# Kernel tuning notes

Measured on AMD Instinct MI355X. Metric: run time of the kernel, lower is better.

Reference implementation:

```python
import jax, jax.numpy as jnp
import numpy as np

D_IN = 32
D_MODEL = 128
B, T = 512, 512
INPUT_DIM = 2 * D_IN  # concat_mask=True, d_u=0


def setup_inputs() -> dict:
    key = jax.random.key(0)
    ks = jax.random.split(key, 8)
    scale = 0.05
    return {
        "x": jax.random.normal(ks[0], (B, T, D_IN), dtype=jnp.float32),
        "W_ih": jax.random.normal(ks[1], (3 * D_MODEL, INPUT_DIM), dtype=jnp.float32) * scale,
        "W_hh": jax.random.normal(ks[2], (3 * D_MODEL, D_MODEL), dtype=jnp.float32) * scale,
        "b_ih": jax.random.normal(ks[3], (3 * D_MODEL,), dtype=jnp.float32) * scale,
        "b_hh": jax.random.normal(ks[4], (3 * D_MODEL,), dtype=jnp.float32) * scale,
        "W_out": jax.random.normal(ks[5], (D_IN, D_MODEL), dtype=jnp.float32) * scale,
        "b_out": jax.random.normal(ks[6], (D_IN,), dtype=jnp.float32) * scale,
        "mask": jax.random.randint(ks[7], (B, T, D_IN), 0, 2, dtype=jnp.int32),
    }


def reference(x, W_ih, W_hh, b_ih, b_hh, W_out, b_out, mask):
    m_bool = mask.astype(bool)                      # [B,T,d_in]
    m_f = mask.astype(x.dtype)
    x = jnp.where(m_bool, x, jnp.zeros_like(x))     # zero-fill missing

    h0 = jnp.zeros((x.shape[0], D_MODEL), dtype=x.dtype)   # state_init='zero'
    x_hat0 = h0 @ W_out.T + b_out                   # readout of initial state

    def gru_cell(x_t, h):
        gx = x_t @ W_ih.T + b_ih                    # [B, 3*d_model]
        gh = h @ W_hh.T + b_hh
        xr, xz, xn = jnp.split(gx, 3, axis=-1)
        hr, hz, hn = jnp.split(gh, 3, axis=-1)
        r = jax.nn.sigmoid(xr + hr)
        z = jax.nn.sigmoid(xz + hz)
        n = jnp.tanh(xn + r * hn)
        return (1.0 - z) * n + z * h

    def step(carry, inp):
        h, x_hat = carry
        x_s, mb_s, mf_s = inp                       # [B,d_in] each
        x_p = jnp.where(mb_s, x_s, x_hat)           # fill blanks with prediction
        x_t = jnp.concatenate([x_p, mf_s], axis=-1) # concat_mask=True
        h_new = gru_cell(x_t, h)
        x_hat_new = h_new @ W_out.T + b_out
        return (h_new, x_hat_new), x_hat_new

    # scan over steps 0..T-2 (time-major)
    xs = jnp.swapaxes(x[:, :-1], 0, 1)              # [T-1, B, d_in]
    mbs = jnp.swapaxes(m_bool[:, :-1], 0, 1)
    mfs = jnp.swapaxes(m_f[:, :-1], 0, 1)
    _, preds = jax.lax.scan(step, (h0, x_hat0), (xs, mbs, mfs))  # [T-1, B, d_in]

    out = jnp.concatenate([x_hat0[None], preds], axis=0)         # [T, B, d_in]
    return jnp.swapaxes(out, 0, 1)                                # [B, T, d_in]
```

## Files before the change

### kernel.cpp

```cpp
#include <hip/hip_runtime.h>
#include <hip/hip_bf16.h>

#define D_IN 32
#define TT 512
#define GB 16
#define NBLK 32
#define MAGIC 0x51F7C0DEu

typedef __attribute__((ext_vector_type(8))) short bf16x8;
typedef __attribute__((ext_vector_type(4))) float f32x4;
typedef __attribute__((ext_vector_type(4))) int   i32x4;
typedef __attribute__((ext_vector_type(2))) unsigned u32x2;

__device__ inline short bf16_of(float f) {
    union { float f; unsigned u; } v; v.f = f;
    unsigned r = v.u + 0x7FFFu + ((v.u >> 16) & 1u);
    return (short)(r >> 16);
}
__device__ inline unsigned cvt_pk_bf16(float lo, float hi) {
    unsigned r;
    asm("v_cvt_pk_bf16_f32 %0, %1, %2" : "=v"(r) : "v"(lo), "v"(hi));
    return r;
}
__device__ inline bf16x8 load8_bf16(const float* __restrict__ p) {
    bf16x8 r;
#pragma unroll
    for (int e = 0; e < 8; ++e) r[e] = bf16_of(p[e]);
    return r;
}
__device__ inline bf16x8 load44_bf16(const float* __restrict__ p, int qq) {
    bf16x8 r;
#pragma unroll
    for (int e = 0; e < 4; ++e) {
        r[e]     = bf16_of(p[qq * 4 + e]);
        r[4 + e] = bf16_of(p[16 + qq * 4 + e]);
    }
    return r;
}
__device__ inline f32x4 splat4(float v) { return (f32x4){v, v, v, v}; }

__device__ inline float sigmoid_fast(float x) {
    return __builtin_amdgcn_rcpf(1.0f + __expf(-x));
}
__device__ inline float tanh_fast(float x) {
    return 1.0f - 2.0f * __builtin_amdgcn_rcpf(__expf(2.0f * x) + 1.0f);
}
__device__ inline void lds_barrier() {
    asm volatile("s_waitcnt lgkmcnt(0)\n\ts_barrier" ::: "memory");
}

__global__ __launch_bounds__(512, 2)
void rnn_imputer(const float* __restrict__ x,
                 const float* __restrict__ W_ih,
                 const float* __restrict__ W_hh,
                 const float* __restrict__ b_ih,
                 const float* __restrict__ b_hh,
                 const float* __restrict__ W_out,
                 const float* __restrict__ b_out,
                 const int*   __restrict__ mask,
                 float* __restrict__ out,
                 unsigned*    flags,
                 int          use_spin) {
    if (blockIdx.x >= NBLK) {
        if (!use_spin || threadIdx.x >= 64) return;
        const unsigned long long t0 = __builtin_amdgcn_s_memrealtime();
        float a0 = 1.0f + threadIdx.x * 1e-6f, a1 = a0 + 0.1f, a2 = a0 + 0.2f,
              a3 = a0 + 0.3f, a4 = a0 + 0.4f, a5 = a0 + 0.5f, a6 = a0 + 0.6f,
              a7 = a0 + 0.7f;
        for (;;) {
            unsigned acc = 0;
#pragma unroll
            for (int j = 0; j < NBLK; ++j)
                acc |= (__hip_atomic_load(&flags[j], __ATOMIC_RELAXED,
                                          __HIP_MEMORY_SCOPE_AGENT) ^ MAGIC);
            if (acc == 0) break;
            if (__builtin_amdgcn_s_memrealtime() - t0 > 200000ull) break;
            for (int i = 0; i < 32; ++i) {
                a0 = __builtin_fmaf(a0, 1.0000001f, 1e-8f);
                a1 = __builtin_fmaf(a1, 1.0000001f, 1e-8f);
                a2 = __builtin_fmaf(a2, 1.0000001f, 1e-8f);
                a3 = __builtin_fmaf(a3, 1.0000001f, 1e-8f);
                a4 = __builtin_fmaf(a4, 1.0000001f, 1e-8f);
                a5 = __builtin_fmaf(a5, 1.0000001f, 1e-8f);
                a6 = __builtin_fmaf(a6, 1.0000001f, 1e-8f);
                a7 = __builtin_fmaf(a7, 1.0000001f, 1e-8f);
            }
            __builtin_amdgcn_s_sleep(24);
        }
        const float s = a0 + a1 + a2 + a3 + a4 + a5 + a6 + a7;
        if (s == 1.2345e30f) ((float*)flags)[NBLK + 1] = s;
        return;
    }

    __shared__ __align__(16) float xch[16][GB][36];
    __shared__ __align__(16) int   mch[16][GB][36];
    __shared__ __align__(16) short hbuf[2][GB][136];
    __shared__ __align__(16) unsigned a0sh[4][16][4];
    __shared__ __align__(16) unsigned a1sh[4][16][4];

    const int tid  = threadIdx.x;
    const int wv   = tid >> 6;
    const int lane = tid & 63;
    const int q    = lane >> 4;
    const int c    = lane & 15;
    const int bb   = blockIdx.x * GB;
    const int brow = bb + c;
    const int i_col = wv * 16 + c;

    bf16x8 Br[6], Bz[6], Bxn[2], Bhn[4];
    Br[0]  = load44_bf16(W_ih + (size_t)i_col * 64, q);
    Br[1]  = load44_bf16(W_ih + (size_t)i_col * 64 + 32, q);
    Bz[0]  = load44_bf16(W_ih + (size_t)(128 + i_col) * 64, q);
    Bz[1]  = load44_bf16(W_ih + (size_t)(128 + i_col) * 64 + 32, q);
    Bxn[0] = load44_bf16(W_ih + (size_t)(256 + i_col) * 64, q);
    Bxn[1] = load44_bf16(W_ih + (size_t)(256 + i_col) * 64 + 32, q);
#pragma unroll
    for (int kt = 2; kt < 6; ++kt) {
        const int k = (kt - 2) * 32 + q * 8;
        Br[kt] = load8_bf16(W_hh + (size_t)i_col * 128 + k);
        Bz[kt] = load8_bf16(W_hh + (size_t)(128 + i_col) * 128 + k);
    }
#pragma unroll
    for (int kt = 0; kt < 4; ++kt)
        Bhn[kt] = load8_bf16(W_hh + (size_t)(256 + i_col) * 128 + kt * 32 + q * 8);

    bf16x8 Ao[2][4];
#pragma unroll
    for (int ta = 0; ta < 2; ++ta)
#pragma unroll
        for (int kt = 0; kt < 4; ++kt)
            Ao[ta][kt] = load8_bf16(W_out + (size_t)(ta * 16 + c) * 128 + kt * 32 + q * 8);

    f32x4 bo_v[2];
#pragma unroll
    for (int ta = 0; ta < 2; ++ta)
        bo_v[ta] = *(const f32x4*)&b_out[ta * 16 + q * 4];

    const float bR  = b_ih[i_col]       + b_hh[i_col];
    const float bZ  = b_ih[128 + i_col] + b_hh[128 + i_col];
    const float bXN = b_ih[256 + i_col];
    const float bHN = b_hh[256 + i_col];

    float h_reg[4] = {0.f, 0.f, 0.f, 0.f};

    bf16x8 A0, A1;
    {
        const size_t o = (size_t)brow * TT * D_IN;
        const f32x4 xa = *(const f32x4*)&x[o + q * 4];
        const f32x4 xb = *(const f32x4*)&x[o + 16 + q * 4];
        const i32x4 ma = *(const i32x4*)&mask[o + q * 4];
        const i32x4 mb = *(const i32x4*)&mask[o + 16 + q * 4];
        union { bf16x8 v; unsigned d[4]; } a0, a1;
#pragma unroll
        for (int j = 0; j < 4; ++j) {
            const float fa = ma[j] ? xa[j] : b_out[q * 4 + j];
            const float fb = mb[j] ? xb[j] : b_out[16 + q * 4 + j];
            ((short*)&a0.v)[j]     = bf16_of(fa);
            ((short*)&a0.v)[4 + j] = bf16_of(fb);
            ((short*)&a1.v)[j]     = ma[j] ? (short)0x3F80 : (short)0;
            ((short*)&a1.v)[4 + j] = mb[j] ? (short)0x3F80 : (short)0;
        }
        A0 = a0.v; A1 = a1.v;
    }
#pragma unroll
    for (int ta = 0; ta < 2; ++ta)
        if (wv == ta)
            *(f32x4*)&out[(size_t)brow * TT * D_IN + ta * 16 + q * 4] = bo_v[ta];

#pragma unroll
    for (int rnd = 0; rnd < 4; ++rnd) {
        const int ts  = 1 + rnd * 4 + (tid >> 7);
        const int row = (tid >> 3) & 15;
        const int c4  = (tid & 7) * 4;
        const size_t o = ((size_t)(bb + row) * TT + ts) * D_IN + c4;
        *(f32x4*)&xch[ts & 15][row][c4] = *(const f32x4*)&x[o];
        *(i32x4*)&mch[ts & 15][row][c4] = *(const i32x4*)&mask[o];
    }

    f32x4 Ra = splat4(bR), Za = splat4(bZ);
    f32x4 Rb = splat4(0.f), Zb = splat4(0.f);
    f32x4 HNa = splat4(bHN), HNb = splat4(0.f);

    f32x4 sgx[2] = {splat4(0.f), splat4(0.f)};
    i32x4 sgm[2] = {(i32x4){0,0,0,0}, (i32x4){0,0,0,0}};

    __syncthreads();

    for (int t = 0; t < TT - 1; ++t) {
        Rb = __builtin_amdgcn_mfma_f32_16x16x32_bf16(A0, Br[0],  Rb, 0, 0, 0);
        Zb = __builtin_amdgcn_mfma_f32_16x16x32_bf16(A0, Bz[0],  Zb, 0, 0, 0);
        f32x4 XNb = __builtin_amdgcn_mfma_f32_16x16x32_bf16(A0, Bxn[0], splat4(0.f), 0, 0, 0);
        Ra = __builtin_amdgcn_mfma_f32_16x16x32_bf16(A1, Br[1],  Ra, 0, 0, 0);
        Za = __builtin_amdgcn_mfma_f32_16x16x32_bf16(A1, Bz[1],  Za, 0, 0, 0);
        f32x4 XNa = __builtin_amdgcn_mfma_f32_16x16x32_bf16(A1, Bxn[1], splat4(bXN), 0, 0, 0);

        const int sl = (t + 1) & 15;
        f32x4 pfx = splat4(0.f);
        i32x4 pfm = (i32x4){0, 0, 0, 0};
        if (wv < 2) {
            pfx = *(const f32x4*)&xch[sl][c][wv * 16 + q * 4];
            pfm = *(const i32x4*)&mch[sl][c][wv * 16 + q * 4];
        }

        if ((t & 7) == 0 && t) {
#pragma unroll
            for (int rnd = 0; rnd < 2; ++rnd) {
                const int tsu = t + 8 + rnd * 4 + (tid >> 7);
                const int row = (tid >> 3) & 15;
                const int c4  = (tid & 7) * 4;
                *(f32x4*)&xch[tsu & 15][row][c4] = sgx[rnd];
                *(i32x4*)&mch[tsu & 15][row][c4] = sgm[rnd];
            }
        }
        if ((t & 7) == 7) {
#pragma unroll
            for (int rnd = 0; rnd < 2; ++rnd) {
                const int tsu = t + 9 + rnd * 4 + (tid >> 7);
                const int ts  = tsu <= TT - 1 ? tsu : TT - 1;
                const int row = (tid >> 3) & 15;
                const int c4  = (tid & 7) * 4;
                const size_t o = ((size_t)(bb + row) * TT + ts) * D_IN + c4;
                sgx[rnd] = *(const f32x4*)&x[o];
                sgm[rnd] = *(const i32x4*)&mask[o];
            }
        }

        const int pb = (t + 1) & 1;
        float hn[4];
#pragma unroll
        for (int r = 0; r < 4; ++r) {
            const float rr = sigmoid_fast(Ra[r] + Rb[r]);
            const float zz = sigmoid_fast(Za[r] + Zb[r]);
            const float nn = tanh_fast(XNa[r] + XNb[r] + rr * (HNa[r] + HNb[r]));
            const float h  = nn + zz * (h_reg[r] - nn);
            h_reg[r] = h;
            hn[r] = h;
        }
        {
            const unsigned pk0 = cvt_pk_bf16(hn[0], hn[1]);
            const unsigned pk1 = cvt_pk_bf16(hn[2], hn[3]);
            hbuf[pb][q * 4 + 0][i_col] = (short)(pk0 & 0xFFFFu);
            hbuf[pb][q * 4 + 1][i_col] = (short)(pk0 >> 16);
            hbuf[pb][q * 4 + 2][i_col] = (short)(pk1 & 0xFFFFu);
            hbuf[pb][q * 4 + 3][i_col] = (short)(pk1 >> 16);
        }

        lds_barrier();

        bf16x8 Ah[4];
#pragma unroll
        for (int kt = 0; kt < 4; ++kt)
            Ah[kt] = *(const bf16x8*)&hbuf[pb][c][kt * 32 + q * 8];

        f32x4 roA = splat4(0.f), roB = splat4(0.f);
        if (wv < 2) {
            roA = __builtin_amdgcn_mfma_f32_16x16x32_bf16(Ao[wv][0], Ah[0], bo_v[wv], 0, 0, 0);
            roB = __builtin_amdgcn_mfma_f32_16x16x32_bf16(Ao[wv][2], Ah[2], splat4(0.f), 0, 0, 0);
            roA = __builtin_amdgcn_mfma_f32_16x16x32_bf16(Ao[wv][1], Ah[1], roA, 0, 0, 0);
            roB = __builtin_amdgcn_mfma_f32_16x16x32_bf16(Ao[wv][3], Ah[3], roB, 0, 0, 0);
        }

        Ra  = __builtin_amdgcn_mfma_f32_16x16x32_bf16(Ah[0], Br[2], splat4(bR), 0, 0, 0);
        Za  = __builtin_amdgcn_mfma_f32_16x16x32_bf16(Ah[0], Bz[2], splat4(bZ), 0, 0, 0);
        HNa = __builtin_amdgcn_mfma_f32_16x16x32_bf16(Ah[0], Bhn[0], splat4(bHN), 0, 0, 0);
        Rb  = __builtin_amdgcn_mfma_f32_16x16x32_bf16(Ah[2], Br[4], splat4(0.f), 0, 0, 0);
        Zb  = __builtin_amdgcn_mfma_f32_16x16x32_bf16(Ah[2], Bz[4], splat4(0.f), 0, 0, 0);
        Ra  = __builtin_amdgcn_mfma_f32_16x16x32_bf16(Ah[1], Br[3], Ra, 0, 0, 0);
        Za  = __builtin_amdgcn_mfma_f32_16x16x32_bf16(Ah[1], Bz[3], Za, 0, 0, 0);
        HNa = __builtin_amdgcn_mfma_f32_16x16x32_bf16(Ah[1], Bhn[1], HNa, 0, 0, 0);
        Rb  = __builtin_amdgcn_mfma_f32_16x16x32_bf16(Ah[3], Br[5], Rb, 0, 0, 0);
        Zb  = __builtin_amdgcn_mfma_f32_16x16x32_bf16(Ah[3], Bz[5], Zb, 0, 0, 0);
        HNb = __builtin_amdgcn_mfma_f32_16x16x32_bf16(Ah[2], Bhn[2], splat4(0.f), 0, 0, 0);
        HNb = __builtin_amdgcn_mfma_f32_16x16x32_bf16(Ah[3], Bhn[3], HNb, 0, 0, 0);

        if (wv < 2) {
            f32x4 xh;
#pragma unroll
            for (int r = 0; r < 4; ++r) xh[r] = roA[r] + roB[r];
            *(f32x4*)&out[((size_t)brow * TT + (t + 1)) * D_IN + wv * 16 + q * 4] = xh;

            const float v0 = pfm[0] ? pfx[0] : xh[0];
            const float v1 = pfm[1] ? pfx[1] : xh[1];
            const float v2 = pfm[2] ? pfx[2] : xh[2];
            const float v3 = pfm[3] ? pfx[3] : xh[3];
            u32x2 pa;
            pa[0] = cvt_pk_bf16(v0, v1);
            pa[1] = cvt_pk_bf16(v2, v3);
            *(u32x2*)&a0sh[q][c][wv * 2] = pa;
            u32x2 pm;
            pm[0] = (pfm[0] ? 0x3F80u : 0u) | ((pfm[1] ? 0x3F80u : 0u) << 16);
            pm[1] = (pfm[2] ? 0x3F80u : 0u) | ((pfm[3] ? 0x3F80u : 0u) << 16);
            *(u32x2*)&a1sh[q][c][wv * 2] = pm;
        }

        lds_barrier();

        A0 = *(const bf16x8*)&a0sh[q][c][0];
        A1 = *(const bf16x8*)&a1sh[q][c][0];
    }

    if (use_spin && tid == 0)
        __hip_atomic_store(&flags[blockIdx.x], MAGIC, __ATOMIC_RELAXED,
                           __HIP_MEMORY_SCOPE_AGENT);
}

extern "C" void kernel_launch(void* const* d_in, const int* in_sizes, int n_in,
                              void* d_out, int out_size, void* d_ws, size_t ws_size,
                              hipStream_t stream) {
    const float* x     = (const float*)d_in[0];
    const float* W_ih  = (const float*)d_in[1];
    const float* W_hh  = (const float*)d_in[2];
    const float* b_ih  = (const float*)d_in[3];
    const float* b_hh  = (const float*)d_in[4];
    const float* W_out = (const float*)d_in[5];
    const float* b_out = (const float*)d_in[6];
    const int*   mask  = (const int*)d_in[7];
    float* out = (float*)d_out;

    const int use_spin = (d_ws != nullptr && ws_size >= 256) ? 1 : 0;
    const int grid = use_spin ? 256 : NBLK;

    rnn_imputer<<<dim3(grid), dim3(512), 0, stream>>>(
        x, W_ih, W_hh, b_ih, b_hh, W_out, b_out, mask, out,
        (unsigned*)d_ws, use_spin);
}
```

Before: 719.3 us.

## Interleave two independent batch groups per block to hide recurrence latency

Each block now processes 32 batch rows as two independent 16-row groups (P and Q), with 16 blocks instead of 32. The GRU gate phase of one group is interleaved with the hidden-projection phase of the other between barriers, so MFMA and transcendental latency of one group can overlap the other's dependent work. The LDS staging ring for x/mask is removed, and the prefetch now loads x and mask straight from global memory every step. This halves the number of blocks, so fewer CUs are used, and the per-step global loads sit on the critical path.

```diff
diff --git a/kernel.cpp b/kernel.cpp
--- a/kernel.cpp
+++ b/kernel.cpp
@@ -3,8 +3,7 @@
 
 #define D_IN 32
 #define TT 512
-#define GB 16
-#define NBLK 32
+#define NBLK 16
 #define MAGIC 0x51F7C0DEu
 
 typedef __attribute__((ext_vector_type(8))) short bf16x8;
@@ -48,6 +47,85 @@
 __device__ inline void lds_barrier() {
     asm volatile("s_waitcnt lgkmcnt(0)\n\ts_barrier" ::: "memory");
 }
+
+#define MFMA16(A, B, C) __builtin_amdgcn_mfma_f32_16x16x32_bf16(A, B, C, 0, 0, 0)
+
+#define PHASE_A(S, isro, ta, brow, pfx, pfm, Ra, Za, Rb, Zb, HNa, HNb, hreg, t_) do { \
+    const bf16x8 A0v_ = *(const bf16x8*)&a0sh[S][q][c][0]; \
+    const bf16x8 A1v_ = *(const bf16x8*)&a1sh[S][q][c][0]; \
+    if (isro) { \
+        const size_t o_ = ((size_t)(brow) * TT + ((t_) + 1)) * D_IN + (ta) * 16 + q * 4; \
+        pfx = *(const f32x4*)&x[o_]; \
+        pfm = *(const i32x4*)&mask[o_]; \
+    } \
+    Rb = MFMA16(A0v_, Br[0], Rb); \
+    Zb = MFMA16(A0v_, Bz[0], Zb); \
+    const f32x4 XNb_ = MFMA16(A0v_, Bxn[0], splat4(0.f)); \
+    Ra = MFMA16(A1v_, Br[1], Ra); \
+    Za = MFMA16(A1v_, Bz[1], Za); \
+    const f32x4 XNa_ = MFMA16(A1v_, Bxn[1], splat4(bXN)); \
+    float hn_[4]; \
+    _Pragma("unroll") \
+    for (int r = 0; r < 4; ++r) { \
+        const float rr_ = sigmoid_fast(Ra[r] + Rb[r]); \
+        const float zz_ = sigmoid_fast(Za[r] + Zb[r]); \
+        const float nn_ = tanh_fast(XNa_[r] + XNb_[r] + rr_ * (HNa[r] + HNb[r])); \
+        const float h_ = nn_ + zz_ * (hreg[r] - nn_); \
+        hreg[r] = h_; hn_[r] = h_; \
+    } \
+    { \
+        const unsigned pk0_ = cvt_pk_bf16(hn_[0], hn_[1]); \
+        const unsigned pk1_ = cvt_pk_bf16(hn_[2], hn_[3]); \
+        hbuf[S][q * 4 + 0][i_col] = (short)(pk0_ & 0xFFFFu); \
+        hbuf[S][q * 4 + 1][i_col] = (short)(pk0_ >> 16); \
+        hbuf[S][q * 4 + 2][i_col] = (short)(pk1_ & 0xFFFFu); \
+        hbuf[S][q * 4 + 3][i_col] = (short)(pk1_ >> 16); \
+    } \
+} while (0)
+
+#define PHASE_B(S, isro, ta, brow, pfx, pfm, Ra, Za, Rb, Zb, HNa, HNb, t_) do { \
+    const bf16x8 Ah0_ = *(const bf16x8*)&hbuf[S][c][0 * 32 + q * 8]; \
+    const bf16x8 Ah1_ = *(const bf16x8*)&hbuf[S][c][1 * 32 + q * 8]; \
+    const bf16x8 Ah2_ = *(const bf16x8*)&hbuf[S][c][2 * 32 + q * 8]; \
+    const bf16x8 Ah3_ = *(const bf16x8*)&hbuf[S][c][3 * 32 + q * 8]; \
+    f32x4 roA_ = splat4(0.f), roB_ = splat4(0.f); \
+    if (isro) { \
+        roA_ = MFMA16(Ao_h[0], Ah0_, bo_h); \
+        roB_ = MFMA16(Ao_h[2], Ah2_, splat4(0.f)); \
+        roA_ = MFMA16(Ao_h[1], Ah1_, roA_); \
+        roB_ = MFMA16(Ao_h[3], Ah3_, roB_); \
+    } \
+    Ra = MFMA16(Ah0_, Br[2], splat4(bR)); \
+    Za = MFMA16(Ah0_, Bz[2], splat4(bZ)); \
+    HNa = MFMA16(Ah0_, Bhn[0], splat4(bHN)); \
+    Rb = MFMA16(Ah2_, Br[4], splat4(0.f)); \
+    Zb = MFMA16(Ah2_, Bz[4], splat4(0.f)); \
+    Ra = MFMA16(Ah1_, Br[3], Ra); \
+    Za = MFMA16(Ah1_, Bz[3], Za); \
+    HNa = MFMA16(Ah1_, Bhn[1], HNa); \
+    Rb = MFMA16(Ah3_, Br[5], Rb); \
+    Zb = MFMA16(Ah3_, Bz[5], Zb); \
+    HNb = MFMA16(Ah2_, Bhn[2], splat4(0.f)); \
+    HNb = MFMA16(Ah3_, Bhn[3], HNb); \
+    if (isro) { \
+        f32x4 xh_; \
+        _Pragma("unroll") \
+        for (int r = 0; r < 4; ++r) xh_[r] = roA_[r] + roB_[r]; \
+        *(f32x4*)&out[((size_t)(brow) * TT + ((t_) + 1)) * D_IN + (ta) * 16 + q * 4] = xh_; \
+        const float v0_ = pfm[0] ? pfx[0] : xh_[0]; \
+        const float v1_ = pfm[1] ? pfx[1] : xh_[1]; \
+        const float v2_ = pfm[2] ? pfx[2] : xh_[2]; \
+        const float v3_ = pfm[3] ? pfx[3] : xh_[3]; \
+        u32x2 pa_; \
+        pa_[0] = cvt_pk_bf16(v0_, v1_); \
+        pa_[1] = cvt_pk_bf16(v2_, v3_); \
+        *(u32x2*)&a0sh[S][q][c][(ta) * 2] = pa_; \
+        u32x2 pm_; \
+        pm_[0] = (pfm[0] ? 0x3F80u : 0u) | ((pfm[1] ? 0x3F80u : 0u) << 16); \
+        pm_[1] = (pfm[2] ? 0x3F80u : 0u) | ((pfm[3] ? 0x3F80u : 0u) << 16); \
+        *(u32x2*)&a1sh[S][q][c][(ta) * 2] = pm_; \
+    } \
+} while (0)
 
 __global__ __launch_bounds__(512, 2)
 void rnn_imputer(const float* __restrict__ x,
@@ -92,20 +170,22 @@
         return;
     }
 
-    __shared__ __align__(16) float xch[16][GB][36];
-    __shared__ __align__(16) int   mch[16][GB][36];
-    __shared__ __align__(16) short hbuf[2][GB][136];
-    __shared__ __align__(16) unsigned a0sh[4][16][4];
-    __shared__ __align__(16) unsigned a1sh[4][16][4];
+    __shared__ __align__(16) short    hbuf[2][16][136];
+    __shared__ __align__(16) unsigned a0sh[2][4][16][4];
+    __shared__ __align__(16) unsigned a1sh[2][4][16][4];
 
     const int tid  = threadIdx.x;
     const int wv   = tid >> 6;
     const int lane = tid & 63;
     const int q    = lane >> 4;
     const int c    = lane & 15;
-    const int bb   = blockIdx.x * GB;
-    const int brow = bb + c;
+    const int bb   = blockIdx.x * 32;
     const int i_col = wv * 16 + c;
+    const int browP = bb + c;
+    const int browQ = bb + 16 + c;
+    const bool roP = (wv < 2);
+    const bool roQ = (wv == 2 || wv == 3);
+    const int  taU = wv & 1;
 
     bf16x8 Br[6], Bz[6], Bxn[2], Bhn[4];
     Br[0]  = load44_bf16(W_ih + (size_t)i_col * 64, q);
@@ -124,180 +204,65 @@
     for (int kt = 0; kt < 4; ++kt)
         Bhn[kt] = load8_bf16(W_hh + (size_t)(256 + i_col) * 128 + kt * 32 + q * 8);
 
-    bf16x8 Ao[2][4];
-#pragma unroll
-    for (int ta = 0; ta < 2; ++ta)
-#pragma unroll
-        for (int kt = 0; kt < 4; ++kt)
-            Ao[ta][kt] = load8_bf16(W_out + (size_t)(ta * 16 + c) * 128 + kt * 32 + q * 8);
-
-    f32x4 bo_v[2];
-#pragma unroll
-    for (int ta = 0; ta < 2; ++ta)
-        bo_v[ta] = *(const f32x4*)&b_out[ta * 16 + q * 4];
+    bf16x8 Ao_h[4];
+#pragma unroll
+    for (int kt = 0; kt < 4; ++kt)
+        Ao_h[kt] = load8_bf16(W_out + (size_t)(taU * 16 + c) * 128 + kt * 32 + q * 8);
+    const f32x4 bo_h = *(const f32x4*)&b_out[taU * 16 + q * 4];
 
     const float bR  = b_ih[i_col]       + b_hh[i_col];
     const float bZ  = b_ih[128 + i_col] + b_hh[128 + i_col];
     const float bXN = b_ih[256 + i_col];
     const float bHN = b_hh[256 + i_col];
 
-    float h_reg[4] = {0.f, 0.f, 0.f, 0.f};
-
-    bf16x8 A0, A1;
-    {
-        const size_t o = (size_t)brow * TT * D_IN;
-        const f32x4 xa = *(const f32x4*)&x[o + q * 4];
-        const f32x4 xb = *(const f32x4*)&x[o + 16 + q * 4];
-        const i32x4 ma = *(const i32x4*)&mask[o + q * 4];
-        const i32x4 mb = *(const i32x4*)&mask[o + 16 + q * 4];
-        union { bf16x8 v; unsigned d[4]; } a0, a1;
-#pragma unroll
-        for (int j = 0; j < 4; ++j) {
-            const float fa = ma[j] ? xa[j] : b_out[q * 4 + j];
-            const float fb = mb[j] ? xb[j] : b_out[16 + q * 4 + j];
-            ((short*)&a0.v)[j]     = bf16_of(fa);
-            ((short*)&a0.v)[4 + j] = bf16_of(fb);
-            ((short*)&a1.v)[j]     = ma[j] ? (short)0x3F80 : (short)0;
-            ((short*)&a1.v)[4 + j] = mb[j] ? (short)0x3F80 : (short)0;
-        }
-        A0 = a0.v; A1 = a1.v;
-    }
-#pragma unroll
-    for (int ta = 0; ta < 2; ++ta)
-        if (wv == ta)
-            *(f32x4*)&out[(size_t)brow * TT * D_IN + ta * 16 + q * 4] = bo_v[ta];
-
-#pragma unroll
-    for (int rnd = 0; rnd < 4; ++rnd) {
-        const int ts  = 1 + rnd * 4 + (tid >> 7);
-        const int row = (tid >> 3) & 15;
-        const int c4  = (tid & 7) * 4;
-        const size_t o = ((size_t)(bb + row) * TT + ts) * D_IN + c4;
-        *(f32x4*)&xch[ts & 15][row][c4] = *(const f32x4*)&x[o];
-        *(i32x4*)&mch[ts & 15][row][c4] = *(const i32x4*)&mask[o];
-    }
-
-    f32x4 Ra = splat4(bR), Za = splat4(bZ);
-    f32x4 Rb = splat4(0.f), Zb = splat4(0.f);
-    f32x4 HNa = splat4(bHN), HNb = splat4(0.f);
-
-    f32x4 sgx[2] = {splat4(0.f), splat4(0.f)};
-    i32x4 sgm[2] = {(i32x4){0,0,0,0}, (i32x4){0,0,0,0}};
-
-    __syncthreads();
-
-    for (int t = 0; t < TT - 1; ++t) {
-        Rb = __builtin_amdgcn_mfma_f32_16x16x32_bf16(A0, Br[0],  Rb, 0, 0, 0);
-        Zb = __builtin_amdgcn_mfma_f32_16x16x32_bf16(A0, Bz[0],  Zb, 0, 0, 0);
-        f32x4 XNb = __builtin_amdgcn_mfma_f32_16x16x32_bf16(A0, Bxn[0], splat4(0.f), 0, 0, 0);
-        Ra = __builtin_amdgcn_mfma_f32_16x16x32_bf16(A1, Br[1],  Ra, 0, 0, 0);
-        Za = __builtin_amdgcn_mfma_f32_16x16x32_bf16(A1, Bz[1],  Za, 0, 0, 0);
-        f32x4 XNa = __builtin_amdgcn_mfma_f32_16x16x32_bf16(A1, Bxn[1], splat4(bXN), 0, 0, 0);
-
-        const int sl = (t + 1) & 15;
-        f32x4 pfx = splat4(0.f);
-        i32x4 pfm = (i32x4){0, 0, 0, 0};
-        if (wv < 2) {
-            pfx = *(const f32x4*)&xch[sl][c][wv * 16 + q * 4];
-            pfm = *(const i32x4*)&mch[sl][c][wv * 16 + q * 4];
-        }
-
-        if ((t & 7) == 0 && t) {
-#pragma unroll
-            for (int rnd = 0; rnd < 2; ++rnd) {
-                const int tsu = t + 8 + rnd * 4 + (tid >> 7);
-                const int row = (tid >> 3) & 15;
-                const int c4  = (tid & 7) * 4;
-                *(f32x4*)&xch[tsu & 15][row][c4] = sgx[rnd];
-                *(i32x4*)&mch[tsu & 15][row][c4] = sgm[rnd];
-            }
-        }
-        if ((t & 7) == 7) {
-#pragma unroll
-            for (int rnd = 0; rnd < 2; ++rnd) {
-                const int tsu = t + 9 + rnd * 4 + (tid >> 7);
-                const int ts  = tsu <= TT - 1 ? tsu : TT - 1;
-                const int row = (tid >> 3) & 15;
-                const int c4  = (tid & 7) * 4;
-                const size_t o = ((size_t)(bb + row) * TT + ts) * D_IN + c4;
-                sgx[rnd] = *(const f32x4*)&x[o];
-                sgm[rnd] = *(const i32x4*)&mask[o];
-            }
-        }
-
-        const int pb = (t + 1) & 1;
-        float hn[4];
-#pragma unroll
-        for (int r = 0; r < 4; ++r) {
-            const float rr = sigmoid_fast(Ra[r] + Rb[r]);
-            const float zz = sigmoid_fast(Za[r] + Zb[r]);
-            const float nn = tanh_fast(XNa[r] + XNb[r] + rr * (HNa[r] + HNb[r]));
-            const float h  = nn + zz * (h_reg[r] - nn);
-            h_reg[r] = h;
-            hn[r] = h;
-        }
-        {
-            const unsigned pk0 = cvt_pk_bf16(hn[0], hn[1]);
-            const unsigned pk1 = cvt_pk_bf16(hn[2], hn[3]);
-            hbuf[pb][q * 4 + 0][i_col] = (short)(pk0 & 0xFFFFu);
-            hbuf[pb][q * 4 + 1][i_col] = (short)(pk0 >> 16);
-            hbuf[pb][q * 4 + 2][i_col] = (short)(pk1 & 0xFFFFu);
-            hbuf[pb][q * 4 + 3][i_col] = (short)(pk1 >> 16);
-        }
-
+    if (wv < 4) {
+        const int  browS = roP ? browP : browQ;
+        const int  S     = roP ? 0 : 1;
+        const size_t o = (size_t)browS * TT * D_IN + taU * 16 + q * 4;
+        const f32x4 xa = *(const f32x4*)&x[o];
+        const i32x4 ma = *(const i32x4*)&mask[o];
+        *(f32x4*)&out[o] = bo_h;
+        const float v0 = ma[0] ? xa[0] : bo_h[0];
+        const float v1 = ma[1] ? xa[1] : bo_h[1];
+        const float v2 = ma[2] ? xa[2] : bo_h[2];
+        const float v3 = ma[3] ? xa[3] : bo_h[3];
+        u32x2 pa;
+        pa[0] = cvt_pk_bf16(v0, v1);
+        pa[1] = cvt_pk_bf16(v2, v3);
+        *(u32x2*)&a0sh[S][q][c][taU * 2] = pa;
+        u32x2 pm;
+        pm[0] = (ma[0] ? 0x3F80u : 0u) | ((ma[1] ? 0x3F80u : 0u) << 16);
+        pm[1] = (ma[2] ? 0x3F80u : 0u) | ((ma[3] ? 0x3F80u : 0u) << 16);
+        *(u32x2*)&a1sh[S][q][c][taU * 2] = pm;
+    }
+
+    f32x4 RaP = splat4(bR), ZaP = splat4(bZ), RbP = splat4(0.f), ZbP = splat4(0.f);
+    f32x4 HNaP = splat4(bHN), HNbP = splat4(0.f);
+    f32x4 RaQ = splat4(bR), ZaQ = splat4(bZ), RbQ = splat4(0.f), ZbQ = splat4(0.f);
+    f32x4 HNaQ = splat4(bHN), HNbQ = splat4(0.f);
+    float hP[4] = {0.f, 0.f, 0.f, 0.f};
+    float hQ[4] = {0.f, 0.f, 0.f, 0.f};
+    f32x4 pfxP = splat4(0.f), pfxQ = splat4(0.f);
+    i32x4 pfmP = (i32x4){0, 0, 0, 0}, pfmQ = (i32x4){0, 0, 0, 0};
+
+    lds_barrier();
+
+    PHASE_A(0, roP, taU, browP, pfxP, pfmP, RaP, ZaP, RbP, ZbP, HNaP, HNbP, hP, 0);
+    lds_barrier();
+    PHASE_B(0, roP, taU, browP, pfxP, pfmP, RaP, ZaP, RbP, ZbP, HNaP, HNbP, 0);
+    PHASE_A(1, roQ, taU, browQ, pfxQ, pfmQ, RaQ, ZaQ, RbQ, ZbQ, HNaQ, HNbQ, hQ, 0);
+    lds_barrier();
+
+    for (int t = 1; t < TT - 1; ++t) {
+        PHASE_A(0, roP, taU, browP, pfxP, pfmP, RaP, ZaP, RbP, ZbP, HNaP, HNbP, hP, t);
+        PHASE_B(1, roQ, taU, browQ, pfxQ, pfmQ, RaQ, ZaQ, RbQ, ZbQ, HNaQ, HNbQ, t - 1);
         lds_barrier();
-
-        bf16x8 Ah[4];
-#pragma unroll
-        for (int kt = 0; kt < 4; ++kt)
-            Ah[kt] = *(const bf16x8*)&hbuf[pb][c][kt * 32 + q * 8];
-
-        f32x4 roA = splat4(0.f), roB = splat4(0.f);
-        if (wv < 2) {
-            roA = __builtin_amdgcn_mfma_f32_16x16x32_bf16(Ao[wv][0], Ah[0], bo_v[wv], 0, 0, 0);
-            roB = __builtin_amdgcn_mfma_f32_16x16x32_bf16(Ao[wv][2], Ah[2], splat4(0.f), 0, 0, 0);
-            roA = __builtin_amdgcn_mfma_f32_16x16x32_bf16(Ao[wv][1], Ah[1], roA, 0, 0, 0);
-            roB = __builtin_amdgcn_mfma_f32_16x16x32_bf16(Ao[wv][3], Ah[3], roB, 0, 0, 0);
-        }
-
-        Ra  = __builtin_amdgcn_mfma_f32_16x16x32_bf16(Ah[0], Br[2], splat4(bR), 0, 0, 0);
-        Za  = __builtin_amdgcn_mfma_f32_16x16x32_bf16(Ah[0], Bz[2], splat4(bZ), 0, 0, 0);
-        HNa = __builtin_amdgcn_mfma_f32_16x16x32_bf16(Ah[0], Bhn[0], splat4(bHN), 0, 0, 0);
-        Rb  = __builtin_amdgcn_mfma_f32_16x16x32_bf16(Ah[2], Br[4], splat4(0.f), 0, 0, 0);
-        Zb  = __builtin_amdgcn_mfma_f32_16x16x32_bf16(Ah[2], Bz[4], splat4(0.f), 0, 0, 0);
-        Ra  = __builtin_amdgcn_mfma_f32_16x16x32_bf16(Ah[1], Br[3], Ra, 0, 0, 0);
-        Za  = __builtin_amdgcn_mfma_f32_16x16x32_bf16(Ah[1], Bz[3], Za, 0, 0, 0);
-        HNa = __builtin_amdgcn_mfma_f32_16x16x32_bf16(Ah[1], Bhn[1], HNa, 0, 0, 0);
-        Rb  = __builtin_amdgcn_mfma_f32_16x16x32_bf16(Ah[3], Br[5], Rb, 0, 0, 0);
-        Zb  = __builtin_amdgcn_mfma_f32_16x16x32_bf16(Ah[3], Bz[5], Zb, 0, 0, 0);
-        HNb = __builtin_amdgcn_mfma_f32_16x16x32_bf16(Ah[2], Bhn[2], splat4(0.f), 0, 0, 0);
-        HNb = __builtin_amdgcn_mfma_f32_16x16x32_bf16(Ah[3], Bhn[3], HNb, 0, 0, 0);
-
-        if (wv < 2) {
-            f32x4 xh;
-#pragma unroll
-            for (int r = 0; r < 4; ++r) xh[r] = roA[r] + roB[r];
-            *(f32x4*)&out[((size_t)brow * TT + (t + 1)) * D_IN + wv * 16 + q * 4] = xh;
-
-            const float v0 = pfm[0] ? pfx[0] : xh[0];
-            const float v1 = pfm[1] ? pfx[1] : xh[1];
-            const float v2 = pfm[2] ? pfx[2] : xh[2];
-            const float v3 = pfm[3] ? pfx[3] : xh[3];
-            u32x2 pa;
-            pa[0] = cvt_pk_bf16(v0, v1);
-            pa[1] = cvt_pk_bf16(v2, v3);
-            *(u32x2*)&a0sh[q][c][wv * 2] = pa;
-            u32x2 pm;
-            pm[0] = (pfm[0] ? 0x3F80u : 0u) | ((pfm[1] ? 0x3F80u : 0u) << 16);
-            pm[1] = (pfm[2] ? 0x3F80u : 0u) | ((pfm[3] ? 0x3F80u : 0u) << 16);
-            *(u32x2*)&a1sh[q][c][wv * 2] = pm;
-        }
-
+        PHASE_B(0, roP, taU, browP, pfxP, pfmP, RaP, ZaP, RbP, ZbP, HNaP, HNbP, t);
+        PHASE_A(1, roQ, taU, browQ, pfxQ, pfmQ, RaQ, ZaQ, RbQ, ZbQ, HNaQ, HNbQ, hQ, t);
         lds_barrier();
-
-        A0 = *(const bf16x8*)&a0sh[q][c][0];
-        A1 = *(const bf16x8*)&a1sh[q][c][0];
-    }
+    }
+
+    PHASE_B(1, roQ, taU, browQ, pfxQ, pfmQ, RaQ, ZaQ, RbQ, ZbQ, HNaQ, HNbQ, TT - 2);
 
     if (use_spin && tid == 0)
         __hip_atomic_store(&flags[blockIdx.x], MAGIC, __ATOMIC_RELAXED,
```

Result: slower. 873.6 us (+21.4%).
